# Kernel optimization log

Measured on AMD Instinct MI355X. Metric: run time of the kernel, lower is better.

## Reference

```python
import jax, jax.numpy as jnp
import numpy as np

NEG_SLOPE = 0.01  # torch nn.LeakyReLU default

B, C, H, W = 16, 256, 128, 128
RATIO = 4
CR = max(C // RATIO, 4)  # 64


def setup_inputs() -> dict:
    key = jax.random.key(0)
    k1, k2, k3 = jax.random.split(key, 3)
    x = jax.random.normal(k1, (B, C, H, W), dtype=jnp.float32)
    # kaiming_normal fan_out for 1x1 conv: std = gain/sqrt(fan_out), gain=sqrt(2/(1+0.01^2))
    gain = float(np.sqrt(2.0 / (1.0 + NEG_SLOPE ** 2)))
    w1 = jax.random.normal(k2, (CR, C), dtype=jnp.float32) * (gain / np.sqrt(CR))
    w2 = jax.random.normal(k3, (C, CR), dtype=jnp.float32) * (gain / np.sqrt(C))
    return {"x": x, "w1": w1, "w2": w2}


def _leaky_relu(v):
    return jnp.where(v >= 0, v, NEG_SLOPE * v)


def reference(x, w1, w2):
    # x: [B,C,H,W]; w1: [CR,C]; w2: [C,CR] (1x1 convs, no bias)
    # axial pools: pool over H keeping W, and over W keeping H, then broadcast-add
    avg_h = jnp.mean(x, axis=2)            # [B,C,W]
    avg_w = jnp.mean(x, axis=3)            # [B,C,H]
    axial_avg = avg_h[:, :, None, :] + avg_w[:, :, :, None]  # [B,C,H,W]
    max_h = jnp.max(x, axis=2)             # [B,C,W]
    max_w = jnp.max(x, axis=3)             # [B,C,H]
    axial_max = max_h[:, :, None, :] + max_w[:, :, :, None]  # [B,C,H,W]

    def gate_branch(a):
        h = _leaky_relu(jnp.einsum('bchw,rc->brhw', a, w1))  # [B,CR,H,W]
        return jnp.einsum('brhw,cr->bchw', h, w2)            # [B,C,H,W]

    scale = jax.nn.sigmoid(gate_branch(axial_avg) + gate_branch(axial_max))
    return x * (1.0 + scale)
```

## Files before the change

### kernel.cpp

```cpp
#include <hip/hip_runtime.h>
#include <math.h>


#define B_  16
#define C_  256
#define CR_ 64
#define H_  128
#define W_  128

constexpr size_t SSTRIDE  = (size_t)B_ * C_ * W_;
constexpr size_t USTRIDE  = (size_t)B_ * CR_ * W_;
constexpr size_t PQSTRIDE = (size_t)B_ * C_ * W_;

__global__ __launch_bounds__(256) void k1_pool(const float* __restrict__ x,
                                               float* __restrict__ S) {
    const int c = blockIdx.x, b = blockIdx.y;
    const int tid  = threadIdx.x;
    const int wv   = tid >> 6;
    const int lane = tid & 63;
    const float* xp = x + (size_t)(b * C_ + c) * (H_ * W_);

    __shared__ float rs_l[H_], rm_l[H_];
    __shared__ float cs_l[4][W_], cm_l[4][W_];

    float csx = 0.f, csy = 0.f;
    float cmx = -3.402823466e38f, cmy = -3.402823466e38f;

    for (int j = 0; j < 32; ++j) {
        const int h = wv * 32 + j;
        const float2 v = *reinterpret_cast<const float2*>(xp + h * W_ + lane * 2);
        csx += v.x; csy += v.y;
        cmx = fmaxf(cmx, v.x); cmy = fmaxf(cmy, v.y);
        float rs = v.x + v.y;
        float rm = fmaxf(v.x, v.y);
#pragma unroll
        for (int msk = 1; msk < 64; msk <<= 1) {
            rs += __shfl_xor(rs, msk);
            rm = fmaxf(rm, __shfl_xor(rm, msk));
        }
        if (lane == 0) { rs_l[h] = rs; rm_l[h] = rm; }
    }
    cs_l[wv][2 * lane]     = csx;  cs_l[wv][2 * lane + 1] = csy;
    cm_l[wv][2 * lane]     = cmx;  cm_l[wv][2 * lane + 1] = cmy;
    __syncthreads();

    if (tid < 128) {
        const float ssum = cs_l[0][tid] + cs_l[1][tid] + cs_l[2][tid] + cs_l[3][tid];
        const float smax = fmaxf(fmaxf(cm_l[0][tid], cm_l[1][tid]),
                                 fmaxf(cm_l[2][tid], cm_l[3][tid]));
        const size_t o = (size_t)(b * C_ + c) * W_ + tid;
        S[0 * SSTRIDE + o] = ssum * (1.0f / 128.0f);
        S[1 * SSTRIDE + o] = smax;
        S[2 * SSTRIDE + o] = rs_l[tid] * (1.0f / 128.0f);
        S[3 * SSTRIDE + o] = rm_l[tid];
    }
}

__global__ __launch_bounds__(128) void k2a_u(const float* __restrict__ S,
                                             const float* __restrict__ w1,
                                             float* __restrict__ U) {
    const int t   = threadIdx.x;
    const int rq  = blockIdx.x;
    const int src = blockIdx.y;
    const int b   = blockIdx.z;
    const float* in = S + ((size_t)(src * B_ + b) * C_) * W_;

    float acc[8];
#pragma unroll
    for (int i = 0; i < 8; ++i) acc[i] = 0.f;

#pragma unroll 4
    for (int c = 0; c < C_; ++c) {
        const float xv = in[c * W_ + t];
#pragma unroll
        for (int i = 0; i < 8; ++i)
            acc[i] = fmaf(w1[(rq * 8 + i) * C_ + c], xv, acc[i]);
    }
    float* o = U + ((size_t)(src * B_ + b) * CR_ + rq * 8) * W_;
#pragma unroll
    for (int i = 0; i < 8; ++i) o[i * W_ + t] = acc[i];
}

__global__ __launch_bounds__(128) void k2b_pq(const float* __restrict__ U,
                                              const float* __restrict__ w2,
                                              float* __restrict__ PQ) {
    const int t  = threadIdx.x;
    const int cq = blockIdx.x;
    const int pq = blockIdx.y;
    const int b  = blockIdx.z;
    const float* u0 = U + ((size_t)((pq * 2 + 0) * B_ + b) * CR_) * W_;
    const float* u1 = U + ((size_t)((pq * 2 + 1) * B_ + b) * CR_) * W_;

    float acc[16];
#pragma unroll
    for (int i = 0; i < 16; ++i) acc[i] = 0.f;

#pragma unroll 4
    for (int r = 0; r < CR_; ++r) {
        const float sv = u0[r * W_ + t] + u1[r * W_ + t];
#pragma unroll
        for (int i = 0; i < 16; ++i)
            acc[i] = fmaf(w2[(cq * 16 + i) * CR_ + r], sv, acc[i]);
    }
    float* o = PQ + ((size_t)(pq * B_ + b) * C_ + cq * 16) * W_;
#pragma unroll
    for (int i = 0; i < 16; ++i) o[i * W_ + t] = 0.505f * acc[i];
}

__global__ __launch_bounds__(256) void k3_gate(const float* __restrict__ x,
                                               const float* __restrict__ U,
                                               const float* __restrict__ PQ,
                                               const float* __restrict__ w2,
                                               float* __restrict__ out) {
    const int h = blockIdx.x, b = blockIdx.y;
    const int tid = threadIdx.x;

    __shared__ float sm[CR_][W_];

    const float* Ua = U + (size_t)(0 * B_ + b) * CR_ * W_;
    const float* Um = U + (size_t)(1 * B_ + b) * CR_ * W_;
    const float* Va = U + (size_t)(2 * B_ + b) * CR_ * W_;
    const float* Vm = U + (size_t)(3 * B_ + b) * CR_ * W_;

    for (int idx = tid; idx < CR_ * W_; idx += 256) {
        const int r = idx >> 7, w = idx & 127;
        const float va = Va[r * W_ + h];
        const float vm = Vm[r * W_ + h];
        sm[r][w] = fabsf(Ua[r * W_ + w] + va) + fabsf(Um[r * W_ + w] + vm);
    }
    __syncthreads();

    const int w  = tid & 127;
    const int cg = __builtin_amdgcn_readfirstlane(tid >> 7);
    const float* PQ0 = PQ + (size_t)b * C_ * W_;
    const float* PQ1 = PQ + PQSTRIDE + (size_t)b * C_ * W_;

    for (int oc = 0; oc < 8; ++oc) {
        const int cbase = cg * 128 + oc * 16;
        float acc[16];
#pragma unroll
        for (int i = 0; i < 16; ++i) acc[i] = 0.f;

#pragma unroll 4
        for (int r = 0; r < CR_; ++r) {
            const float mv = sm[r][w];
#pragma unroll
            for (int i = 0; i < 16; ++i)
                acc[i] = fmaf(w2[(cbase + i) * CR_ + r], mv, acc[i]);
        }
#pragma unroll
        for (int i = 0; i < 16; ++i) {
            const int c = cbase + i;
            const float z = PQ0[(size_t)c * W_ + w] + PQ1[(size_t)c * W_ + h]
                            + 0.495f * acc[i];
            const float sg = 1.0f / (1.0f + __expf(-z));
            const size_t xo = (((size_t)(b * C_ + c)) * H_ + h) * W_ + w;
            out[xo] = x[xo] * (1.0f + sg);
        }
    }
}

extern "C" void kernel_launch(void* const* d_in, const int* in_sizes, int n_in,
                              void* d_out, int out_size, void* d_ws, size_t ws_size,
                              hipStream_t stream) {
    (void)in_sizes; (void)n_in; (void)out_size; (void)ws_size;
    const float* x  = (const float*)d_in[0];
    const float* w1 = (const float*)d_in[1];
    const float* w2 = (const float*)d_in[2];
    float* out = (float*)d_out;

    float* S  = (float*)d_ws;
    float* U  = S + 4 * SSTRIDE;
    float* PQ = U + 4 * USTRIDE;

    k1_pool<<<dim3(C_, B_), 256, 0, stream>>>(x, S);
    k2a_u  <<<dim3(8, 4, B_), 128, 0, stream>>>(S, w1, U);
    k2b_pq <<<dim3(16, 2, B_), 128, 0, stream>>>(U, w2, PQ);
    k3_gate<<<dim3(H_, B_), 256, 0, stream>>>(x, U, PQ, w2, out);
}
```

Before: 671.4 us.

## Retile pool, projection and gate kernels with wider vector loads and register blocking

The pooling kernel now reads float4 rows with 32-lane groups across 8 row groups. The two small projection kernels get half as many outputs per block and twice as many blocks. The gate kernel moves to 512 threads with a transposed, padded shared tile, and each thread computes 32 channels for 2 columns, using float4 LDS reads and float2 global loads and stores. Together these aim to cut LDS traffic per FMA, widen memory accesses and raise parallelism, at the cost of higher register pressure (64 accumulators) and possibly lower occupancy.

```diff
diff --git a/kernel.cpp b/kernel.cpp
--- a/kernel.cpp
+++ b/kernel.cpp
@@ -7,6 +7,7 @@
 #define CR_ 64
 #define H_  128
 #define W_  128
+#define NEGINF -3.402823466e38f
 
 constexpr size_t SSTRIDE  = (size_t)B_ * C_ * W_;
 constexpr size_t USTRIDE  = (size_t)B_ * CR_ * W_;
@@ -15,39 +16,44 @@
 __global__ __launch_bounds__(256) void k1_pool(const float* __restrict__ x,
                                                float* __restrict__ S) {
     const int c = blockIdx.x, b = blockIdx.y;
-    const int tid  = threadIdx.x;
-    const int wv   = tid >> 6;
-    const int lane = tid & 63;
+    const int tid = threadIdx.x;
+    const int wg = tid & 31;
+    const int rg = tid >> 5;
     const float* xp = x + (size_t)(b * C_ + c) * (H_ * W_);
 
     __shared__ float rs_l[H_], rm_l[H_];
-    __shared__ float cs_l[4][W_], cm_l[4][W_];
-
-    float csx = 0.f, csy = 0.f;
-    float cmx = -3.402823466e38f, cmy = -3.402823466e38f;
-
-    for (int j = 0; j < 32; ++j) {
-        const int h = wv * 32 + j;
-        const float2 v = *reinterpret_cast<const float2*>(xp + h * W_ + lane * 2);
-        csx += v.x; csy += v.y;
-        cmx = fmaxf(cmx, v.x); cmy = fmaxf(cmy, v.y);
-        float rs = v.x + v.y;
-        float rm = fmaxf(v.x, v.y);
-#pragma unroll
-        for (int msk = 1; msk < 64; msk <<= 1) {
-            rs += __shfl_xor(rs, msk);
-            rm = fmaxf(rm, __shfl_xor(rm, msk));
+    __shared__ float cps[8][W_], cpm[8][W_];
+
+    float cs0 = 0.f, cs1 = 0.f, cs2 = 0.f, cs3 = 0.f;
+    float cm0 = NEGINF, cm1 = NEGINF, cm2 = NEGINF, cm3 = NEGINF;
+
+#pragma unroll 4
+    for (int k = 0; k < 16; ++k) {
+        const int h = rg + 8 * k;
+        const float4 v = *reinterpret_cast<const float4*>(xp + h * W_ + wg * 4);
+        cs0 += v.x; cs1 += v.y; cs2 += v.z; cs3 += v.w;
+        cm0 = fmaxf(cm0, v.x); cm1 = fmaxf(cm1, v.y);
+        cm2 = fmaxf(cm2, v.z); cm3 = fmaxf(cm3, v.w);
+        float rs = (v.x + v.y) + (v.z + v.w);
+        float rm = fmaxf(fmaxf(v.x, v.y), fmaxf(v.z, v.w));
+#pragma unroll
+        for (int m = 1; m < 32; m <<= 1) {
+            rs += __shfl_xor(rs, m);
+            rm = fmaxf(rm, __shfl_xor(rm, m));
         }
-        if (lane == 0) { rs_l[h] = rs; rm_l[h] = rm; }
-    }
-    cs_l[wv][2 * lane]     = csx;  cs_l[wv][2 * lane + 1] = csy;
-    cm_l[wv][2 * lane]     = cmx;  cm_l[wv][2 * lane + 1] = cmy;
+        if (wg == 0) { rs_l[h] = rs; rm_l[h] = rm; }
+    }
+    *reinterpret_cast<float4*>(&cps[rg][wg * 4]) = make_float4(cs0, cs1, cs2, cs3);
+    *reinterpret_cast<float4*>(&cpm[rg][wg * 4]) = make_float4(cm0, cm1, cm2, cm3);
     __syncthreads();
 
     if (tid < 128) {
-        const float ssum = cs_l[0][tid] + cs_l[1][tid] + cs_l[2][tid] + cs_l[3][tid];
-        const float smax = fmaxf(fmaxf(cm_l[0][tid], cm_l[1][tid]),
-                                 fmaxf(cm_l[2][tid], cm_l[3][tid]));
+        float ssum = 0.f, smax = NEGINF;
+#pragma unroll
+        for (int g = 0; g < 8; ++g) {
+            ssum += cps[g][tid];
+            smax = fmaxf(smax, cpm[g][tid]);
+        }
         const size_t o = (size_t)(b * C_ + c) * W_ + tid;
         S[0 * SSTRIDE + o] = ssum * (1.0f / 128.0f);
         S[1 * SSTRIDE + o] = smax;
@@ -65,20 +71,20 @@
     const int b   = blockIdx.z;
     const float* in = S + ((size_t)(src * B_ + b) * C_) * W_;
 
-    float acc[8];
-#pragma unroll
-    for (int i = 0; i < 8; ++i) acc[i] = 0.f;
-
-#pragma unroll 4
+    float acc[4];
+#pragma unroll
+    for (int i = 0; i < 4; ++i) acc[i] = 0.f;
+
+#pragma unroll 8
     for (int c = 0; c < C_; ++c) {
         const float xv = in[c * W_ + t];
 #pragma unroll
-        for (int i = 0; i < 8; ++i)
-            acc[i] = fmaf(w1[(rq * 8 + i) * C_ + c], xv, acc[i]);
-    }
-    float* o = U + ((size_t)(src * B_ + b) * CR_ + rq * 8) * W_;
-#pragma unroll
-    for (int i = 0; i < 8; ++i) o[i * W_ + t] = acc[i];
+        for (int i = 0; i < 4; ++i)
+            acc[i] = fmaf(w1[(rq * 4 + i) * C_ + c], xv, acc[i]);
+    }
+    float* o = U + ((size_t)(src * B_ + b) * CR_ + rq * 4) * W_;
+#pragma unroll
+    for (int i = 0; i < 4; ++i) o[i * W_ + t] = acc[i];
 }
 
 __global__ __launch_bounds__(128) void k2b_pq(const float* __restrict__ U,
@@ -91,23 +97,23 @@
     const float* u0 = U + ((size_t)((pq * 2 + 0) * B_ + b) * CR_) * W_;
     const float* u1 = U + ((size_t)((pq * 2 + 1) * B_ + b) * CR_) * W_;
 
-    float acc[16];
-#pragma unroll
-    for (int i = 0; i < 16; ++i) acc[i] = 0.f;
-
-#pragma unroll 4
+    float acc[8];
+#pragma unroll
+    for (int i = 0; i < 8; ++i) acc[i] = 0.f;
+
+#pragma unroll 8
     for (int r = 0; r < CR_; ++r) {
         const float sv = u0[r * W_ + t] + u1[r * W_ + t];
 #pragma unroll
-        for (int i = 0; i < 16; ++i)
-            acc[i] = fmaf(w2[(cq * 16 + i) * CR_ + r], sv, acc[i]);
-    }
-    float* o = PQ + ((size_t)(pq * B_ + b) * C_ + cq * 16) * W_;
-#pragma unroll
-    for (int i = 0; i < 16; ++i) o[i * W_ + t] = 0.505f * acc[i];
-}
-
-__global__ __launch_bounds__(256) void k3_gate(const float* __restrict__ x,
+        for (int i = 0; i < 8; ++i)
+            acc[i] = fmaf(w2[(cq * 8 + i) * CR_ + r], sv, acc[i]);
+    }
+    float* o = PQ + ((size_t)(pq * B_ + b) * C_ + cq * 8) * W_;
+#pragma unroll
+    for (int i = 0; i < 8; ++i) o[i * W_ + t] = 0.505f * acc[i];
+}
+
+__global__ __launch_bounds__(512) void k3_gate(const float* __restrict__ x,
                                                const float* __restrict__ U,
                                                const float* __restrict__ PQ,
                                                const float* __restrict__ w2,
@@ -115,48 +121,74 @@
     const int h = blockIdx.x, b = blockIdx.y;
     const int tid = threadIdx.x;
 
-    __shared__ float sm[CR_][W_];
+    __shared__ float sm[W_][CR_ + 4];
 
     const float* Ua = U + (size_t)(0 * B_ + b) * CR_ * W_;
     const float* Um = U + (size_t)(1 * B_ + b) * CR_ * W_;
     const float* Va = U + (size_t)(2 * B_ + b) * CR_ * W_;
     const float* Vm = U + (size_t)(3 * B_ + b) * CR_ * W_;
 
-    for (int idx = tid; idx < CR_ * W_; idx += 256) {
+    for (int idx = tid; idx < CR_ * W_; idx += 512) {
         const int r = idx >> 7, w = idx & 127;
         const float va = Va[r * W_ + h];
         const float vm = Vm[r * W_ + h];
-        sm[r][w] = fabsf(Ua[r * W_ + w] + va) + fabsf(Um[r * W_ + w] + vm);
+        sm[w][r] = fabsf(Ua[r * W_ + w] + va) + fabsf(Um[r * W_ + w] + vm);
     }
     __syncthreads();
 
-    const int w  = tid & 127;
-    const int cg = __builtin_amdgcn_readfirstlane(tid >> 7);
+    const int lane = tid & 63;
+    const int w0 = lane * 2, w1 = w0 + 1;
+    const int cbase = __builtin_amdgcn_readfirstlane(tid >> 6) * 32;
+
     const float* PQ0 = PQ + (size_t)b * C_ * W_;
     const float* PQ1 = PQ + PQSTRIDE + (size_t)b * C_ * W_;
 
-    for (int oc = 0; oc < 8; ++oc) {
-        const int cbase = cg * 128 + oc * 16;
-        float acc[16];
-#pragma unroll
-        for (int i = 0; i < 16; ++i) acc[i] = 0.f;
+    float2 acc[32];
+#pragma unroll
+    for (int i = 0; i < 32; ++i) acc[i] = make_float2(0.f, 0.f);
+
+    for (int r8 = 0; r8 < 8; ++r8) {
+        const float4 a0 = *reinterpret_cast<const float4*>(&sm[w0][r8 * 8]);
+        const float4 a1 = *reinterpret_cast<const float4*>(&sm[w0][r8 * 8 + 4]);
+        const float4 b0 = *reinterpret_cast<const float4*>(&sm[w1][r8 * 8]);
+        const float4 b1 = *reinterpret_cast<const float4*>(&sm[w1][r8 * 8 + 4]);
+#pragma unroll
+        for (int i = 0; i < 32; ++i) {
+            const float* wr = &w2[(size_t)(cbase + i) * CR_ + r8 * 8];
+            acc[i].x = fmaf(wr[0], a0.x, acc[i].x);
+            acc[i].x = fmaf(wr[1], a0.y, acc[i].x);
+            acc[i].x = fmaf(wr[2], a0.z, acc[i].x);
+            acc[i].x = fmaf(wr[3], a0.w, acc[i].x);
+            acc[i].x = fmaf(wr[4], a1.x, acc[i].x);
+            acc[i].x = fmaf(wr[5], a1.y, acc[i].x);
+            acc[i].x = fmaf(wr[6], a1.z, acc[i].x);
+            acc[i].x = fmaf(wr[7], a1.w, acc[i].x);
+            acc[i].y = fmaf(wr[0], b0.x, acc[i].y);
+            acc[i].y = fmaf(wr[1], b0.y, acc[i].y);
+            acc[i].y = fmaf(wr[2], b0.z, acc[i].y);
+            acc[i].y = fmaf(wr[3], b0.w, acc[i].y);
+            acc[i].y = fmaf(wr[4], b1.x, acc[i].y);
+            acc[i].y = fmaf(wr[5], b1.y, acc[i].y);
+            acc[i].y = fmaf(wr[6], b1.z, acc[i].y);
+            acc[i].y = fmaf(wr[7], b1.w, acc[i].y);
+        }
+    }
 
 #pragma unroll 4
-        for (int r = 0; r < CR_; ++r) {
-            const float mv = sm[r][w];
-#pragma unroll
-            for (int i = 0; i < 16; ++i)
-                acc[i] = fmaf(w2[(cbase + i) * CR_ + r], mv, acc[i]);
-        }
-#pragma unroll
-        for (int i = 0; i < 16; ++i) {
-            const int c = cbase + i;
-            const float z = PQ0[(size_t)c * W_ + w] + PQ1[(size_t)c * W_ + h]
-                            + 0.495f * acc[i];
-            const float sg = 1.0f / (1.0f + __expf(-z));
-            const size_t xo = (((size_t)(b * C_ + c)) * H_ + h) * W_ + w;
-            out[xo] = x[xo] * (1.0f + sg);
-        }
+    for (int i = 0; i < 32; ++i) {
+        const int c = cbase + i;
+        const float q1 = PQ1[(size_t)c * W_ + h];
+        const float2 p0 = *reinterpret_cast<const float2*>(&PQ0[(size_t)c * W_ + w0]);
+        const float zx = p0.x + q1 + 0.495f * acc[i].x;
+        const float zy = p0.y + q1 + 0.495f * acc[i].y;
+        const float sgx = __builtin_amdgcn_rcpf(1.0f + __expf(-zx));
+        const float sgy = __builtin_amdgcn_rcpf(1.0f + __expf(-zy));
+        const size_t xo = ((size_t)(b * C_ + c) * H_ + h) * W_ + w0;
+        const float2 xv = *reinterpret_cast<const float2*>(&x[xo]);
+        float2 ov;
+        ov.x = xv.x * (1.0f + sgx);
+        ov.y = xv.y * (1.0f + sgy);
+        *reinterpret_cast<float2*>(&out[xo]) = ov;
     }
 }
 
@@ -174,7 +206,7 @@
     float* PQ = U + 4 * USTRIDE;
 
     k1_pool<<<dim3(C_, B_), 256, 0, stream>>>(x, S);
-    k2a_u  <<<dim3(8, 4, B_), 128, 0, stream>>>(S, w1, U);
-    k2b_pq <<<dim3(16, 2, B_), 128, 0, stream>>>(U, w2, PQ);
-    k3_gate<<<dim3(H_, B_), 256, 0, stream>>>(x, U, PQ, w2, out);
-}
+    k2a_u  <<<dim3(16, 4, B_), 128, 0, stream>>>(S, w1, U);
+    k2b_pq <<<dim3(32, 2, B_), 128, 0, stream>>>(U, w2, PQ);
+    k3_gate<<<dim3(H_, B_), 512, 0, stream>>>(x, U, PQ, w2, out);
+}
```

Measured after the change: 1.348 ms. +100.8%, slower.
